# Kernel optimization log

Hardware: AMD Instinct MI355X
Metric: run time of the kernel (lower is better)

Reference implementation:

```python
import jax, jax.numpy as jnp
import numpy as np

N_NODES = 20000
N_EDGES = 200000
NC = 32          # node feature dim (nfeat)
FDIM = 13        # edge feature dim
FHID = 64        # filter-net hidden dim
NREPEATS = 10


def setup_inputs() -> dict:
    key = jax.random.key(0)
    ks = jax.random.split(key, 12)
    s = 1.0 / np.sqrt(NC)
    return {
        "hx": jax.random.normal(ks[0], (N_NODES, NC), jnp.float32),
        "edge_index": jax.random.randint(ks[1], (2, N_EDGES), 0, N_NODES, jnp.int32),
        "edge_feats": jax.random.normal(ks[2], (N_EDGES, FDIM), jnp.float32),
        # filter generating network (weight-shared across iterations)
        "fW1": jax.random.normal(ks[3], (FDIM, FHID), jnp.float32) / np.sqrt(FDIM),
        "fb1": jnp.zeros((FHID,), jnp.float32),
        "fW2": jax.random.normal(ks[4], (FHID, NC * NC), jnp.float32) / np.sqrt(FHID),
        "fb2": jnp.zeros((NC * NC,), jnp.float32),
        # GRU cell params (torch.nn.GRUCell layout: gates r, z, n)
        "Wi": jax.random.uniform(ks[5], (NC, 3 * NC), jnp.float32, -s, s),
        "Wh": jax.random.uniform(ks[6], (NC, 3 * NC), jnp.float32, -s, s),
        "bi": jax.random.uniform(ks[7], (3 * NC,), jnp.float32, -s, s),
        "bh": jax.random.uniform(ks[8], (3 * NC,), jnp.float32, -s, s),
    }


def _gru_cell(x, h, Wi, Wh, bi, bh):
    gi = x @ Wi + bi
    gh = h @ Wh + bh
    ir, iz, inn = jnp.split(gi, 3, axis=1)
    hr, hz, hn = jnp.split(gh, 3, axis=1)
    r = jax.nn.sigmoid(ir + hr)
    z = jax.nn.sigmoid(iz + hz)
    n = jnp.tanh(inn + r * hn)
    return (1.0 - z) * n + z * h


def reference(hx, edge_index, edge_feats, fW1, fb1, fW2, fb2, Wi, Wh, bi, bh):
    n_nodes, nc = hx.shape
    src, dst = edge_index[0], edge_index[1]
    # filter net: per-edge [nc, nc] weight matrices, shared over iterations
    h1 = jax.nn.relu(edge_feats @ fW1 + fb1)
    weights = (h1 @ fW2 + fb2).reshape(-1, nc, nc)  # [E, in, out]
    # degree normalization for scatter-mean aggregation (ECC semantics)
    deg = jax.ops.segment_sum(jnp.ones_like(dst, jnp.float32), dst, num_segments=n_nodes)
    inv_deg = (1.0 / jnp.maximum(deg, 1.0))[:, None]  # [N,1]

    hxs = [hx]
    for _ in range(NREPEATS):
        # gather src feats, per-edge matvec, scatter-mean into dst
        msg = jnp.einsum("ei,eio->eo", hx[src], weights)            # [E, nc]
        agg = jax.ops.segment_sum(msg, dst, num_segments=n_nodes) * inv_deg
        hx = _gru_cell(agg, hx, Wi, Wh, bi, bh)
        hxs.append(hx)
    return jnp.concatenate(hxs, axis=1)  # cat_all=True -> [N, nc*(nrepeats+1)]
```

## Files before the change

### kernel.cpp

```cpp
#include <hip/hip_runtime.h>
#include <hip/hip_bf16.h>

#define NNODES 20000
#define NEDGES 200000
#define NCD 32
#define FDIMD 13
#define FHIDD 64
#define NREPD 10
#define OUTCD (NCD * (NREPD + 1))
#define NCT 130
#define NPB 8
#define NBLK (NNODES / NPB)
#define MAXTILES 40000
#define YKST 72
#define YNST (32 * YKST)

typedef short bf16x8 __attribute__((ext_vector_type(8)));
typedef float f32x4 __attribute__((ext_vector_type(4)));

__global__ __launch_bounds__(256) void k_copy_h0(const float* __restrict__ hx,
                                                 float* __restrict__ out,
                                                 __hip_bfloat16* __restrict__ hxb) {
    int tid = blockIdx.x * 256 + threadIdx.x;
    if (tid < NNODES * NCD) {
        float v = hx[tid];
        out[(size_t)(tid >> 5) * OUTCD + (tid & 31)] = v;
        hxb[tid] = __float2bfloat16(v);
    }
}

__global__ __launch_bounds__(256) void k_degrees(const int* __restrict__ ei,
                                                 float* __restrict__ indeg,
                                                 int* __restrict__ outcnt) {
    int e = blockIdx.x * 256 + threadIdx.x;
    if (e < NEDGES) {
        atomicAdd(&indeg[ei[NEDGES + e]], 1.0f);
        atomicAdd(&outcnt[ei[e]], 1);
    }
}

__global__ __launch_bounds__(256) void k_scan(const int* __restrict__ in,
                                              int* __restrict__ out, int n) {
    __shared__ int s_w[4];
    __shared__ int s_base;
    int t = threadIdx.x;
    if (t == 0) s_base = 0;
    __syncthreads();
    for (int base = 0; base < n; base += 256) {
        int i = base + t;
        int v = (i < n) ? in[i] : 0;
        int x = v;
        #pragma unroll
        for (int d = 1; d < 64; d <<= 1) {
            int y = __shfl_up(x, d);
            if ((t & 63) >= d) x += y;
        }
        if ((t & 63) == 63) s_w[t >> 6] = x;
        __syncthreads();
        int wid = t >> 6, wb = 0;
        for (int w = 0; w < wid; ++w) wb += s_w[w];
        if (i < n) out[i] = s_base + wb + x - v;
        int ctot = s_w[0] + s_w[1] + s_w[2] + s_w[3];
        __syncthreads();
        if (t == 0) s_base += ctot;
        __syncthreads();
    }
    if (t == 0) out[n] = s_base;
}

__global__ __launch_bounds__(256) void k_fill(const int* __restrict__ ei,
                                              const int* __restrict__ csr_off,
                                              int* __restrict__ cursor,
                                              int* __restrict__ rank) {
    int e = blockIdx.x * 256 + threadIdx.x;
    if (e < NEDGES) {
        int s = ei[e];
        int p = atomicAdd(&cursor[s], 1);
        rank[e] = csr_off[s] + p;
    }
}

__global__ __launch_bounds__(256) void k_reord(const int* __restrict__ ei,
                                               const int* __restrict__ rank,
                                               int* __restrict__ dsts) {
    int e = blockIdx.x * 256 + threadIdx.x;
    if (e < NEDGES) dsts[rank[e]] = ei[NEDGES + e];
}

__global__ __launch_bounds__(256) void k_tcnt(const int* __restrict__ csr_off,
                                              int* __restrict__ tcnt) {
    int b = blockIdx.x * 256 + threadIdx.x;
    if (b < NBLK) {
        int s = 0;
        for (int j = 0; j < NPB; ++j) {
            int d = csr_off[b * NPB + j + 1] - csr_off[b * NPB + j];
            s += (d + 15) >> 4;
        }
        tcnt[b] = s;
    }
}

__global__ __launch_bounds__(256) void k_tfill(const int* __restrict__ csr_off,
                                               const int* __restrict__ tile_off,
                                               unsigned* __restrict__ tiles) {
    int b = blockIdx.x * 256 + threadIdx.x;
    if (b < NBLK) {
        int off = tile_off[b];
        for (int j = 0; j < NPB; ++j) {
            int s0 = csr_off[b * NPB + j];
            int d  = csr_off[b * NPB + j + 1] - s0;
            for (int q = 0; q < d; q += 16) {
                int cnt = d - q; if (cnt > 16) cnt = 16;
                tiles[off++] = ((unsigned)(s0 + q) << 8) | ((unsigned)cnt << 3) | (unsigned)j;
            }
        }
    }
}

__global__ __launch_bounds__(256) void k_h1(const float* __restrict__ ef,
                                            const float* __restrict__ fW1,
                                            const float* __restrict__ fb1,
                                            const int* __restrict__ rank,
                                            __hip_bfloat16* __restrict__ h1s) {
    __shared__ float s_w1[FDIMD * FHIDD];
    __shared__ float s_ef[4 * FDIMD];
    __shared__ int s_rk[4];
    int t = threadIdx.x;
    for (int idx = t; idx < FDIMD * FHIDD; idx += 256) s_w1[idx] = fW1[idx];
    if (t < 4 * FDIMD) s_ef[t] = ef[(size_t)blockIdx.x * 4 * FDIMD + t];
    if (t < 4) s_rk[t] = rank[blockIdx.x * 4 + t];
    __syncthreads();
    int je = t >> 6, k = t & 63;
    float v = fb1[k];
    #pragma unroll
    for (int j = 0; j < FDIMD; ++j) v += s_ef[je * FDIMD + j] * s_w1[j * FHIDD + k];
    h1s[(size_t)s_rk[je] * FHIDD + k] = __float2bfloat16(fmaxf(v, 0.f));
}

__global__ __launch_bounds__(256) void k_w2frag(const float* __restrict__ fW2,
                                                const float* __restrict__ fb2,
                                                __hip_bfloat16* __restrict__ W2f) {
    int idx = blockIdx.x * 256 + threadIdx.x;
    if (idx >= NCT * 64) return;
    int ct = idx >> 6, lane = idx & 63;
    int j = ct * 16 + (lane & 15);
    __align__(16) __hip_bfloat16 tmp[8];
    #pragma unroll
    for (int jj = 0; jj < 8; ++jj) {
        int i = (lane >> 4) * 8 + jj;
        float v = (j < 2048) ? fW2[(size_t)(j >> 5) * 1024 + i * 32 + (j & 31)]
                             : fb2[i * 32 + (j - 2048)];
        tmp[jj] = __float2bfloat16(v);
    }
    *reinterpret_cast<uint4*>(&W2f[(size_t)ct * 1024 + lane * 8]) =
        *reinterpret_cast<const uint4*>(tmp);
}

__global__ __launch_bounds__(256) void k_prep(const float* __restrict__ Wi,
                                              const float* __restrict__ Wh,
                                              float* __restrict__ WiT,
                                              float* __restrict__ WhT) {
    int idx = blockIdx.x * 256 + threadIdx.x;
    if (idx < 3072) {
        int g = idx >> 5, i = idx & 31;
        WiT[idx] = Wi[i * 96 + g];
        WhT[idx] = Wh[i * 96 + g];
    }
}

__global__ __launch_bounds__(256) void k_msg(
    const int* __restrict__ tile_off, const unsigned* __restrict__ tiles,
    const int* __restrict__ dsts, const __hip_bfloat16* __restrict__ h1s,
    const __hip_bfloat16* __restrict__ hxb, const __hip_bfloat16* __restrict__ W2f,
    float* __restrict__ agg) {
    __shared__ __align__(16) unsigned short sY[NPB * YNST];
    __shared__ float s_bias[NPB][32];
    const int t = threadIdx.x, lane = t & 63, wave = t >> 6;
    const int bid = blockIdx.x;
    const int t0 = tile_off[bid], t1 = tile_off[bid + 1];
    if (t0 == t1) return;
    const int n0 = bid * NPB;

    const int arow = (lane & 15) < NPB ? (lane & 15) : (NPB - 1);
    bf16x8 a = *reinterpret_cast<const bf16x8*>(
        hxb + (size_t)(n0 + arow) * NCD + (lane >> 4) * 8);
    const int colw = lane & 15, rbase = (lane >> 4) * 4;
    for (int ct = wave; ct < NCT; ct += 4) {
        bf16x8 b = *reinterpret_cast<const bf16x8*>(W2f + (size_t)ct * 1024 + lane * 8);
        f32x4 c = {0.f, 0.f, 0.f, 0.f};
        c = __builtin_amdgcn_mfma_f32_16x16x32_bf16(a, b, c, 0, 0, 0);
        if (rbase < NPB) {
            const int j = ct * 16 + colw;
            if (j < 2048) {
                const int k = j >> 5, o = j & 31;
                #pragma unroll
                for (int r = 0; r < 4; ++r)
                    sY[(rbase + r) * YNST + o * YKST + k] =
                        __bfloat16_as_ushort(__float2bfloat16(c[r]));
            } else {
                const int o = j - 2048;
                #pragma unroll
                for (int r = 0; r < 4; ++r) s_bias[rbase + r][o] = c[r];
            }
        }
    }
    __syncthreads();

    const int oc = lane & 15, ks = lane >> 4;
    for (int ti = t0 + wave; ti < t1; ti += 4) {
        const unsigned T = tiles[ti];
        const int start = (int)(T >> 8);
        const int cnt   = (int)((T >> 3) & 31);
        const int row   = (int)(T & 7);
        long eidx = start + oc;
        if (eidx > NEDGES - 1) eidx = NEDGES - 1;
        const bf16x8 a0 = *reinterpret_cast<const bf16x8*>(h1s + eidx * 64 + ks * 8);
        const bf16x8 a1 = *reinterpret_cast<const bf16x8*>(h1s + eidx * 64 + 32 + ks * 8);
        #pragma unroll
        for (int ct = 0; ct < 2; ++ct) {
            const int o = ct * 16 + oc;
            const unsigned short* yp = sY + row * YNST + o * YKST;
            const bf16x8 b0 = *reinterpret_cast<const bf16x8*>(yp + ks * 8);
            const bf16x8 b1 = *reinterpret_cast<const bf16x8*>(yp + 32 + ks * 8);
            const float bias = s_bias[row][o];
            f32x4 acc = {bias, bias, bias, bias};
            acc = __builtin_amdgcn_mfma_f32_16x16x32_bf16(a0, b0, acc, 0, 0, 0);
            acc = __builtin_amdgcn_mfma_f32_16x16x32_bf16(a1, b1, acc, 0, 0, 0);
            #pragma unroll
            for (int r = 0; r < 4; ++r) {
                const int slot = ks * 4 + r;
                if (slot < cnt)
                    atomicAdd(&agg[(size_t)dsts[start + slot] * NCD + o], acc[r]);
            }
        }
    }
}

__global__ __launch_bounds__(256) void k_gru(
    const float* __restrict__ agg, const float* __restrict__ indeg,
    const float* __restrict__ WiT, const float* __restrict__ WhT,
    const float* __restrict__ bi, const float* __restrict__ bh,
    float* __restrict__ out, __hip_bfloat16* __restrict__ hxb, int r) {
    __shared__ __align__(16) float sWiT[96 * 36];
    __shared__ __align__(16) float sWhT[96 * 36];
    __shared__ float s_x[8][32];
    __shared__ float s_h[8][32];
    const int t = threadIdx.x;
    const float4* WiT4 = reinterpret_cast<const float4*>(WiT);
    const float4* WhT4 = reinterpret_cast<const float4*>(WhT);
    for (int p = t; p < 768; p += 256) {
        int g = p >> 3, i = (p & 7) * 4;
        *reinterpret_cast<float4*>(&sWiT[g * 36 + i]) = WiT4[p];
        *reinterpret_cast<float4*>(&sWhT[g * 36 + i]) = WhT4[p];
    }
    const int tid = blockIdx.x * 256 + t;
    const int n   = tid >> 5;
    const int c   = t & 31;
    const int ln  = t >> 5;
    {
        const float invd = 1.0f / fmaxf(indeg[n], 1.0f);
        s_x[ln][c] = agg[(size_t)n * NCD + c] * invd;
        s_h[ln][c] = out[(size_t)n * OUTCD + r * NCD + c];
    }
    __syncthreads();
    float ir = bi[c], iz = bi[NCD + c], in_ = bi[2 * NCD + c];
    float hr = bh[c], hz = bh[NCD + c], hn = bh[2 * NCD + c];
    const float* wi_r = &sWiT[c * 36];
    const float* wi_z = &sWiT[(NCD + c) * 36];
    const float* wi_n = &sWiT[(2 * NCD + c) * 36];
    const float* wh_r = &sWhT[c * 36];
    const float* wh_z = &sWhT[(NCD + c) * 36];
    const float* wh_n = &sWhT[(2 * NCD + c) * 36];
    #pragma unroll
    for (int i4 = 0; i4 < 8; ++i4) {
        const float4 xx = *reinterpret_cast<const float4*>(&s_x[ln][i4 * 4]);
        const float4 hh = *reinterpret_cast<const float4*>(&s_h[ln][i4 * 4]);
        const float4 a = *reinterpret_cast<const float4*>(&wi_r[i4 * 4]);
        const float4 b = *reinterpret_cast<const float4*>(&wi_z[i4 * 4]);
        const float4 g = *reinterpret_cast<const float4*>(&wi_n[i4 * 4]);
        const float4 d = *reinterpret_cast<const float4*>(&wh_r[i4 * 4]);
        const float4 e = *reinterpret_cast<const float4*>(&wh_z[i4 * 4]);
        const float4 f = *reinterpret_cast<const float4*>(&wh_n[i4 * 4]);
        ir  += xx.x * a.x + xx.y * a.y + xx.z * a.z + xx.w * a.w;
        iz  += xx.x * b.x + xx.y * b.y + xx.z * b.z + xx.w * b.w;
        in_ += xx.x * g.x + xx.y * g.y + xx.z * g.z + xx.w * g.w;
        hr  += hh.x * d.x + hh.y * d.y + hh.z * d.z + hh.w * d.w;
        hz  += hh.x * e.x + hh.y * e.y + hh.z * e.z + hh.w * e.w;
        hn  += hh.x * f.x + hh.y * f.y + hh.z * f.z + hh.w * f.w;
    }
    const float rg = 1.f / (1.f + expf(-(ir + hr)));
    const float zg = 1.f / (1.f + expf(-(iz + hz)));
    const float ng = tanhf(in_ + rg * hn);
    const float hv = (1.f - zg) * ng + zg * s_h[ln][c];
    out[(size_t)n * OUTCD + (r + 1) * NCD + c] = hv;
    hxb[(size_t)n * NCD + c] = __float2bfloat16(hv);
}

extern "C" void kernel_launch(void* const* d_in, const int* in_sizes, int n_in,
                              void* d_out, int out_size, void* d_ws, size_t ws_size,
                              hipStream_t stream) {
    const float* hx  = (const float*)d_in[0];
    const int*   ei  = (const int*)d_in[1];
    const float* ef  = (const float*)d_in[2];
    const float* fW1 = (const float*)d_in[3];
    const float* fb1 = (const float*)d_in[4];
    const float* fW2 = (const float*)d_in[5];
    const float* fb2 = (const float*)d_in[6];
    const float* Wi  = (const float*)d_in[7];
    const float* Wh  = (const float*)d_in[8];
    const float* bi  = (const float*)d_in[9];
    const float* bh  = (const float*)d_in[10];
    float* out = (float*)d_out;

    char* ws = (char*)d_ws;
    size_t off = 0;
    auto take = [&](size_t bytes) -> void* {
        void* p = ws + off;
        off = (off + bytes + 255) & ~(size_t)255;
        return p;
    };
    __hip_bfloat16* h1s = (__hip_bfloat16*)take((size_t)NEDGES * FHIDD * 2);
    __hip_bfloat16* hxb = (__hip_bfloat16*)take((size_t)NNODES * NCD * 2);
    __hip_bfloat16* W2f = (__hip_bfloat16*)take((size_t)NCT * 1024 * 2);
    float* agg     = (float*)take((size_t)NNODES * NCD * 4);
    float* indeg   = (float*)take((size_t)NNODES * 4);
    int*   outcnt  = (int*)take((size_t)NNODES * 4);
    int*   csr_off = (int*)take((size_t)(NNODES + 1) * 4);
    int*   cursor  = (int*)take((size_t)NNODES * 4);
    int*   rank    = (int*)take((size_t)NEDGES * 4);
    int*   dsts    = (int*)take((size_t)NEDGES * 4);
    int*   tcnt    = (int*)take((size_t)NBLK * 4);
    int*   tile_off= (int*)take((size_t)(NBLK + 1) * 4);
    unsigned* tiles= (unsigned*)take((size_t)MAXTILES * 4);
    float* WiT     = (float*)take(3072 * 4);
    float* WhT     = (float*)take(3072 * 4);

    hipMemsetAsync(indeg,  0, (size_t)NNODES * 4, stream);
    hipMemsetAsync(outcnt, 0, (size_t)NNODES * 4, stream);
    hipMemsetAsync(cursor, 0, (size_t)NNODES * 4, stream);
    k_copy_h0<<<(NNODES * NCD) / 256, 256, 0, stream>>>(hx, out, hxb);
    k_degrees<<<(NEDGES + 255) / 256, 256, 0, stream>>>(ei, indeg, outcnt);
    k_scan<<<1, 256, 0, stream>>>(outcnt, csr_off, NNODES);
    k_fill<<<(NEDGES + 255) / 256, 256, 0, stream>>>(ei, csr_off, cursor, rank);
    k_reord<<<(NEDGES + 255) / 256, 256, 0, stream>>>(ei, rank, dsts);
    k_tcnt<<<(NBLK + 255) / 256, 256, 0, stream>>>(csr_off, tcnt);
    k_scan<<<1, 256, 0, stream>>>(tcnt, tile_off, NBLK);
    k_tfill<<<(NBLK + 255) / 256, 256, 0, stream>>>(csr_off, tile_off, tiles);
    k_h1<<<NEDGES / 4, 256, 0, stream>>>(ef, fW1, fb1, rank, h1s);
    k_w2frag<<<(NCT * 64 + 255) / 256, 256, 0, stream>>>(fW2, fb2, W2f);
    k_prep<<<12, 256, 0, stream>>>(Wi, Wh, WiT, WhT);

    for (int r = 0; r < NREPD; ++r) {
        hipMemsetAsync(agg, 0, (size_t)NNODES * NCD * 4, stream);
        k_msg<<<NBLK, 256, 0, stream>>>(tile_off, tiles, dsts, h1s, hxb, W2f, agg);
        k_gru<<<(NNODES * NCD) / 256, 256, 0, stream>>>(agg, indeg, WiT, WhT, bi, bh, out, hxb, r);
    }
}
```

Before: 1.027 ms.

## Replace atomic scatter with CSC-ordered message buffer reduced in GRU kernel

Message kernel now writes each edge's bf16 message into a destination-sorted (CSC) slot instead of doing float atomicAdds into agg. The GRU kernel then sums each node's incoming messages sequentially, and the per-iteration memset of agg is dropped. Nodes per block also drops from 8 to 4, which doubles the number of message-kernel blocks. The cost is an extra scan and a CSC position pass at setup, plus bf16 rounding of messages before they are summed, which lowers accuracy.

```diff
diff --git a/kernel.cpp b/kernel.cpp
--- a/kernel.cpp
+++ b/kernel.cpp
@@ -9,7 +9,7 @@
 #define NREPD 10
 #define OUTCD (NCD * (NREPD + 1))
 #define NCT 130
-#define NPB 8
+#define NPB 4
 #define NBLK (NNODES / NPB)
 #define MAXTILES 40000
 #define YKST 72
@@ -31,10 +31,13 @@
 
 __global__ __launch_bounds__(256) void k_degrees(const int* __restrict__ ei,
                                                  float* __restrict__ indeg,
+                                                 int* __restrict__ incnt,
                                                  int* __restrict__ outcnt) {
     int e = blockIdx.x * 256 + threadIdx.x;
     if (e < NEDGES) {
-        atomicAdd(&indeg[ei[NEDGES + e]], 1.0f);
+        int d = ei[NEDGES + e];
+        atomicAdd(&indeg[d], 1.0f);
+        atomicAdd(&incnt[d], 1);
         atomicAdd(&outcnt[ei[e]], 1);
     }
 }
@@ -80,11 +83,17 @@
     }
 }
 
-__global__ __launch_bounds__(256) void k_reord(const int* __restrict__ ei,
-                                               const int* __restrict__ rank,
-                                               int* __restrict__ dsts) {
+__global__ __launch_bounds__(256) void k_cpos(const int* __restrict__ ei,
+                                              const int* __restrict__ rank,
+                                              const int* __restrict__ csc_off,
+                                              int* __restrict__ csc_cur,
+                                              int* __restrict__ cscpos) {
     int e = blockIdx.x * 256 + threadIdx.x;
-    if (e < NEDGES) dsts[rank[e]] = ei[NEDGES + e];
+    if (e < NEDGES) {
+        int dst = ei[NEDGES + e];
+        int p = atomicAdd(&csc_cur[dst], 1);
+        cscpos[rank[e]] = csc_off[dst] + p;
+    }
 }
 
 __global__ __launch_bounds__(256) void k_tcnt(const int* __restrict__ csr_off,
@@ -170,9 +179,9 @@
 
 __global__ __launch_bounds__(256) void k_msg(
     const int* __restrict__ tile_off, const unsigned* __restrict__ tiles,
-    const int* __restrict__ dsts, const __hip_bfloat16* __restrict__ h1s,
+    const int* __restrict__ cscpos, const __hip_bfloat16* __restrict__ h1s,
     const __hip_bfloat16* __restrict__ hxb, const __hip_bfloat16* __restrict__ W2f,
-    float* __restrict__ agg) {
+    __hip_bfloat16* __restrict__ msgC) {
     __shared__ __align__(16) unsigned short sY[NPB * YNST];
     __shared__ float s_bias[NPB][32];
     const int t = threadIdx.x, lane = t & 63, wave = t >> 6;
@@ -216,6 +225,12 @@
         if (eidx > NEDGES - 1) eidx = NEDGES - 1;
         const bf16x8 a0 = *reinterpret_cast<const bf16x8*>(h1s + eidx * 64 + ks * 8);
         const bf16x8 a1 = *reinterpret_cast<const bf16x8*>(h1s + eidx * 64 + 32 + ks * 8);
+        int cp[4];
+        #pragma unroll
+        for (int r = 0; r < 4; ++r) {
+            const int slot = ks * 4 + r;
+            cp[r] = (slot < cnt) ? cscpos[start + slot] : -1;
+        }
         #pragma unroll
         for (int ct = 0; ct < 2; ++ct) {
             const int o = ct * 16 + oc;
@@ -227,17 +242,16 @@
             acc = __builtin_amdgcn_mfma_f32_16x16x32_bf16(a0, b0, acc, 0, 0, 0);
             acc = __builtin_amdgcn_mfma_f32_16x16x32_bf16(a1, b1, acc, 0, 0, 0);
             #pragma unroll
-            for (int r = 0; r < 4; ++r) {
-                const int slot = ks * 4 + r;
-                if (slot < cnt)
-                    atomicAdd(&agg[(size_t)dsts[start + slot] * NCD + o], acc[r]);
-            }
+            for (int r = 0; r < 4; ++r)
+                if (cp[r] >= 0)
+                    msgC[(size_t)cp[r] * NCD + o] = __float2bfloat16(acc[r]);
         }
     }
 }
 
 __global__ __launch_bounds__(256) void k_gru(
-    const float* __restrict__ agg, const float* __restrict__ indeg,
+    const __hip_bfloat16* __restrict__ msgC, const int* __restrict__ csc_off,
+    const float* __restrict__ indeg,
     const float* __restrict__ WiT, const float* __restrict__ WhT,
     const float* __restrict__ bi, const float* __restrict__ bh,
     float* __restrict__ out, __hip_bfloat16* __restrict__ hxb, int r) {
@@ -258,8 +272,12 @@
     const int c   = t & 31;
     const int ln  = t >> 5;
     {
+        const int e0 = csc_off[n], e1 = csc_off[n + 1];
+        float s = 0.f;
+        for (int e = e0; e < e1; ++e)
+            s += __bfloat162float(msgC[(size_t)e * NCD + c]);
         const float invd = 1.0f / fmaxf(indeg[n], 1.0f);
-        s_x[ln][c] = agg[(size_t)n * NCD + c] * invd;
+        s_x[ln][c] = s * invd;
         s_h[ln][c] = out[(size_t)n * OUTCD + r * NCD + c];
     }
     __syncthreads();
@@ -319,30 +337,32 @@
         off = (off + bytes + 255) & ~(size_t)255;
         return p;
     };
-    __hip_bfloat16* h1s = (__hip_bfloat16*)take((size_t)NEDGES * FHIDD * 2);
-    __hip_bfloat16* hxb = (__hip_bfloat16*)take((size_t)NNODES * NCD * 2);
-    __hip_bfloat16* W2f = (__hip_bfloat16*)take((size_t)NCT * 1024 * 2);
-    float* agg     = (float*)take((size_t)NNODES * NCD * 4);
-    float* indeg   = (float*)take((size_t)NNODES * 4);
-    int*   outcnt  = (int*)take((size_t)NNODES * 4);
+    __hip_bfloat16* h1s  = (__hip_bfloat16*)take((size_t)NEDGES * FHIDD * 2);
+    __hip_bfloat16* hxb  = (__hip_bfloat16*)take((size_t)NNODES * NCD * 2);
+    __hip_bfloat16* W2f  = (__hip_bfloat16*)take((size_t)NCT * 1024 * 2);
+    __hip_bfloat16* msgC = (__hip_bfloat16*)take((size_t)NEDGES * NCD * 2);
+    float* indeg   = (float*)take((size_t)NNODES * 4 * 5);
+    int*   outcnt  = (int*)(indeg + NNODES);
+    int*   incnt   = (int*)(indeg + 2 * NNODES);
+    int*   cursor  = (int*)(indeg + 3 * NNODES);
+    int*   csc_cur = (int*)(indeg + 4 * NNODES);
     int*   csr_off = (int*)take((size_t)(NNODES + 1) * 4);
-    int*   cursor  = (int*)take((size_t)NNODES * 4);
+    int*   csc_off = (int*)take((size_t)(NNODES + 1) * 4);
     int*   rank    = (int*)take((size_t)NEDGES * 4);
-    int*   dsts    = (int*)take((size_t)NEDGES * 4);
+    int*   cscpos  = (int*)take((size_t)NEDGES * 4);
     int*   tcnt    = (int*)take((size_t)NBLK * 4);
     int*   tile_off= (int*)take((size_t)(NBLK + 1) * 4);
     unsigned* tiles= (unsigned*)take((size_t)MAXTILES * 4);
     float* WiT     = (float*)take(3072 * 4);
     float* WhT     = (float*)take(3072 * 4);
 
-    hipMemsetAsync(indeg,  0, (size_t)NNODES * 4, stream);
-    hipMemsetAsync(outcnt, 0, (size_t)NNODES * 4, stream);
-    hipMemsetAsync(cursor, 0, (size_t)NNODES * 4, stream);
+    hipMemsetAsync(indeg, 0, (size_t)NNODES * 4 * 5, stream);
     k_copy_h0<<<(NNODES * NCD) / 256, 256, 0, stream>>>(hx, out, hxb);
-    k_degrees<<<(NEDGES + 255) / 256, 256, 0, stream>>>(ei, indeg, outcnt);
+    k_degrees<<<(NEDGES + 255) / 256, 256, 0, stream>>>(ei, indeg, incnt, outcnt);
     k_scan<<<1, 256, 0, stream>>>(outcnt, csr_off, NNODES);
+    k_scan<<<1, 256, 0, stream>>>(incnt, csc_off, NNODES);
     k_fill<<<(NEDGES + 255) / 256, 256, 0, stream>>>(ei, csr_off, cursor, rank);
-    k_reord<<<(NEDGES + 255) / 256, 256, 0, stream>>>(ei, rank, dsts);
+    k_cpos<<<(NEDGES + 255) / 256, 256, 0, stream>>>(ei, rank, csc_off, csc_cur, cscpos);
     k_tcnt<<<(NBLK + 255) / 256, 256, 0, stream>>>(csr_off, tcnt);
     k_scan<<<1, 256, 0, stream>>>(tcnt, tile_off, NBLK);
     k_tfill<<<(NBLK + 255) / 256, 256, 0, stream>>>(csr_off, tile_off, tiles);
@@ -351,8 +371,8 @@
     k_prep<<<12, 256, 0, stream>>>(Wi, Wh, WiT, WhT);
 
     for (int r = 0; r < NREPD; ++r) {
-        hipMemsetAsync(agg, 0, (size_t)NNODES * NCD * 4, stream);
-        k_msg<<<NBLK, 256, 0, stream>>>(tile_off, tiles, dsts, h1s, hxb, W2f, agg);
-        k_gru<<<(NNODES * NCD) / 256, 256, 0, stream>>>(agg, indeg, WiT, WhT, bi, bh, out, hxb, r);
-    }
-}
+        k_msg<<<NBLK, 256, 0, stream>>>(tile_off, tiles, cscpos, h1s, hxb, W2f, msgC);
+        k_gru<<<(NNODES * NCD) / 256, 256, 0, stream>>>(msgC, csc_off, indeg, WiT, WhT,
+                                                        bi, bh, out, hxb, r);
+    }
+}
```

New measurement: 1.136 ms. 1.11x slower.
